# Optimization experiments

Measured on AMD Instinct MI355X. Metric: run time of the kernel, lower is better.

## Reference

```python
import jax, jax.numpy as jnp
import numpy as np

# SparseSphereConv (graph_level=6 -> V=40962, kernel_size=9, stride=1, select_index=None)
# Pipeline: neighbor gather -> data-dependent nonzero row selection ->
# per-vertex KxK interpolation matmul -> 1xK conv (linear over C_in,K) -> scatter back.
# With stride=1 / select_index=None the static selection is the identity, so the
# dynamic nonzero selection is equivalent to computing all rows and zeroing the
# rows whose gathered features are entirely zero (selected rows are scattered back,
# unselected rows stay 0 in sparse_reset's zero-initialized output).

BS, C_IN, C_OUT, V, K = 4, 32, 32, 40962, 9

def setup_inputs() -> dict:
    key = jax.random.key(0)
    k1, k2, k3, k4, k5 = jax.random.split(key, 5)
    x = jax.random.normal(k1, (BS, C_IN, V), dtype=jnp.float32)
    index = jax.random.randint(k2, (V, K), 0, V, dtype=jnp.int32)          # neighbor ids per vertex
    itp_mat = jax.random.uniform(k3, (V, K, K), dtype=jnp.float32)         # per-vertex interpolation
    conv_w = jax.random.normal(k4, (C_OUT, C_IN, K), dtype=jnp.float32) * 0.05  # Conv2d(C_in,C_out,(1,K)) weight
    conv_b = jax.random.normal(k5, (C_OUT,), dtype=jnp.float32) * 0.05
    return {"x": x, "index": index, "itp_mat": itp_mat, "conv_w": conv_w, "conv_b": conv_b}

def reference(x, index, itp_mat, conv_w, conv_b):
    # x: [bs, C, V] -> permute(2,0,1) -> gather neighbors -> [V, K, bs, C]
    g = jnp.transpose(x, (2, 0, 1))[index]
    g = jnp.transpose(g, (3, 2, 0, 1))                      # [C, bs, V, K]  (== reshape of [C, bs*V, K])
    # sparse_prepare: keep rows whose min or max over (C, K) is nonzero (detached in torch)
    gd = jax.lax.stop_gradient(g)
    rmin = gd.min(axis=(0, 3))                              # [bs, V]
    rmax = gd.max(axis=(0, 3))                              # [bs, V]
    mask = (rmin != 0) | (rmax != 0)                        # [bs, V]
    # Interploate: [C, S, 1, K] @ [S, K, K] per row -> batched small matmul
    interp = jnp.einsum('cbvk,vkj->cbvj', g, itp_mat)       # [C, bs, V, K]
    # Conv2d with kernel (1, K): contraction over (C_in, K) + bias
    out = jnp.einsum('cbvk,ock->bov', interp, conv_w) + conv_b[None, :, None]  # [bs, C_out, V]
    # sparse_reset: rows not selected stay zero
    return out * mask[:, None, :].astype(out.dtype)
```

## Files before the change

kernel.cpp:

```cpp
#include <hip/hip_runtime.h>
#include <hip/hip_bf16.h>

#define NV 40962
#define NK 9
#define CIN 32
#define COUT 32
#define NT 2561
#define NV81 (NV * 81)
#define NV9  (NV * 9)

typedef __attribute__((ext_vector_type(8))) short bf16x8;
typedef __attribute__((ext_vector_type(4))) float f32x4;
typedef __attribute__((ext_vector_type(2))) float f32x2;

#define PKFMA_L(A, G, R) asm("v_pk_fma_f32 %0, %1, %2, %0 op_sel:[0,0,0] op_sel_hi:[0,1,1]" : "+v"(A) : "v"(G), "v"(R))
#define PKFMA_H(A, G, R) asm("v_pk_fma_f32 %0, %1, %2, %0 op_sel:[1,0,0] op_sel_hi:[1,1,1]" : "+v"(A) : "v"(G), "v"(R))
#define PKMUL_L(A, G, R) asm("v_pk_mul_f32 %0, %1, %2 op_sel:[0,0] op_sel_hi:[0,1]" : "=v"(A) : "v"(G), "v"(R))
#define PKMUL_H(A, G, R) asm("v_pk_mul_f32 %0, %1, %2 op_sel:[1,0] op_sel_hi:[1,1]" : "=v"(A) : "v"(G), "v"(R))

#define ACC(cc, j) ((j) == 8 ? acc8[cc] : (((j) & 1) ? acc2[cc][(j) >> 1].y \
                                                     : acc2[cc][(j) >> 1].x))

__device__ __forceinline__ unsigned pkbf(float a, float b) {
    union { __hip_bfloat162 h2; unsigned u; } cv;
    cv.h2 = __float22bfloat162_rn(make_float2(a, b));
    return cv.u;
}

__global__ void __launch_bounds__(256) transpose_x_bf16(
    const float* __restrict__ x, unsigned* __restrict__ xtw,
    const float* __restrict__ w, unsigned short* __restrict__ wbf)
{
    __shared__ unsigned U[64 * 65];
    const int t = threadIdx.x;

    const int ci = blockIdx.x * 256 + t;
    if (ci < COUT * CIN * NK) {
        const int o = ci / 288;
        const int r = ci - o * 288;
        const int c = r / 9;
        const int j = r - c * 9;
        unsigned u = __float_as_uint(w[ci]);
        wbf[o * 288 + j * 32 + c] =
            (unsigned short)((u + 0x7FFFu + ((u >> 16) & 1u)) >> 16);
    }

    const int v0  = blockIdx.x * 64;
    const int l16 = t & 15;
    const int p   = t >> 4;

    #pragma unroll
    for (int i = 0; i < 4; ++i) {
        const int q    = p * 4 + i;
        const int r0   = 2 * q;
        const int bb   = r0 >> 5;
        const int c0   = r0 & 31;
        const int dwb  = (c0 >> 3) * 16 + bb * 4 + ((c0 & 7) >> 1);
        const float* rowA = x + (size_t)r0 * NV + v0;
        const float* rowB = rowA + NV;
        #pragma unroll
        for (int hv = 0; hv < 2; ++hv) {
            const int v = l16 * 2 + hv * 32;
            float2 a = make_float2(0.f, 0.f), c2 = make_float2(0.f, 0.f);
            if (v0 + v < NV) {
                a  = *(const float2*)(rowA + v);
                c2 = *(const float2*)(rowB + v);
            }
            U[(v    ) * 65 + dwb] = pkbf(a.x, c2.x);
            U[(v + 1) * 65 + dwb] = pkbf(a.y, c2.y);
        }
    }
    __syncthreads();

    const int v  = t >> 2;
    const int qo = t & 3;
    if (v0 + v < NV) {
        #pragma unroll
        for (int j = 0; j < 4; ++j) {
            const int n = j * 4 + qo;
            uint4 d;
            d.x = U[v * 65 + n * 4 + 0];
            d.y = U[v * 65 + n * 4 + 1];
            d.z = U[v * 65 + n * 4 + 2];
            d.w = U[v * 65 + n * 4 + 3];
            *(uint4*)&xtw[(size_t)(v0 + v) * 64 + n * 4] = d;
        }
    }
}

__global__ void __launch_bounds__(256, 2) sparse_conv_mfma(
    const unsigned short* __restrict__ xt, const int* __restrict__ index,
    const float* __restrict__ itp, const unsigned short* __restrict__ wbf,
    const float* __restrict__ bias, float* __restrict__ out)
{
    __shared__ float itp_s[4][4][108];

    const int t    = threadIdx.x;
    const int w    = t >> 6;
    const int lane = t & 63;
    const int arow = lane & 15;
    const int coct = lane >> 4;
    const int b    = (lane >> 2) & 3;
    const int vv   = lane & 3;
    const int tile = blockIdx.x;

    int ia = tile * 144 + w * 36 + (lane < 36 ? lane : 35);
    ia = ia < NV9 ? ia : NV9 - 1;
    const int myidx = index[ia];

    float iv[6];
    const size_t ibase = (size_t)(tile * 16 + w * 4) * 81;
    #pragma unroll
    for (int i = 0; i < 6; ++i) {
        const int o = i * 64 + lane;
        iv[i] = (o < 324 && ibase + o < (size_t)NV81) ? itp[ibase + o] : 0.0f;
    }

    const unsigned short* wb0 = wbf + arow * 288 + coct * 8;
    uint4 wa0[NK], wa1[NK];
    #pragma unroll
    for (int ks = 0; ks < NK; ++ks) {
        wa0[ks] = *(const uint4*)(wb0 + ks * 32);
        wa1[ks] = *(const uint4*)(wb0 + 16 * 288 + ks * 32);
    }

    float bs0[4], bs1[4];
    #pragma unroll
    for (int r = 0; r < 4; ++r) {
        bs0[r] = bias[coct * 4 + r];
        bs1[r] = bias[coct * 4 + 16 + r];
    }

    int nbr[NK];
    #pragma unroll
    for (int n = 0; n < NK; ++n) nbr[n] = __shfl(myidx, vv * 9 + n);
    const unsigned short* gbase = xt + coct * 32 + b * 8;
    uint4 g[NK];
    #pragma unroll
    for (int n = 0; n < NK; ++n)
        g[n] = *(const uint4*)(gbase + (size_t)nbr[n] * 128);

    #pragma unroll
    for (int i = 0; i < 6; ++i) {
        const int o = i * 64 + lane;
        if (o < 324) {
            const int vloc = o / 81;
            const int r2   = o - vloc * 81;
            const int kk   = r2 / 9;
            const int jj   = r2 - kk * 9;
            itp_s[w][vloc][kk * 12 + jj] = iv[i];
        }
    }
    __builtin_amdgcn_wave_barrier();

    unsigned frag[9][4];
    unsigned nzbits = 0;
    #pragma unroll
    for (int n = 0; n < NK; ++n)
        nzbits |= (g[n].x | g[n].y | g[n].z | g[n].w);
    nzbits &= 0x7FFF7FFFu;

    const float* ib = &itp_s[w][vv][0];
    #pragma unroll
    for (int h = 0; h < 2; ++h) {
        f32x2 acc2[4][4];
        float acc8[4];
        #pragma unroll
        for (int n = 0; n < NK; ++n) {
            const uint2 gk = h ? make_uint2(g[n].z, g[n].w)
                               : make_uint2(g[n].x, g[n].y);
            f32x2 gp01, gp23;
            gp01.x = __uint_as_float(gk.x << 16);
            gp01.y = __uint_as_float(gk.x & 0xFFFF0000u);
            gp23.x = __uint_as_float(gk.y << 16);
            gp23.y = __uint_as_float(gk.y & 0xFFFF0000u);
            const float* ir = ib + n * 12;
            const f32x4 ra = *(const f32x4*)ir;
            const f32x4 rb = *(const f32x4*)(ir + 4);
            const float r8 = ir[8];
            f32x2 rp[4];
            rp[0] = __builtin_shufflevector(ra, ra, 0, 1);
            rp[1] = __builtin_shufflevector(ra, ra, 2, 3);
            rp[2] = __builtin_shufflevector(rb, rb, 0, 1);
            rp[3] = __builtin_shufflevector(rb, rb, 2, 3);
            if (n == 0) {
                #pragma unroll
                for (int jp = 0; jp < 4; ++jp) {
                    PKMUL_L(acc2[0][jp], gp01, rp[jp]);
                    PKMUL_H(acc2[1][jp], gp01, rp[jp]);
                    PKMUL_L(acc2[2][jp], gp23, rp[jp]);
                    PKMUL_H(acc2[3][jp], gp23, rp[jp]);
                }
                acc8[0] = gp01.x * r8; acc8[1] = gp01.y * r8;
                acc8[2] = gp23.x * r8; acc8[3] = gp23.y * r8;
            } else {
                #pragma unroll
                for (int jp = 0; jp < 4; ++jp) {
                    PKFMA_L(acc2[0][jp], gp01, rp[jp]);
                    PKFMA_H(acc2[1][jp], gp01, rp[jp]);
                    PKFMA_L(acc2[2][jp], gp23, rp[jp]);
                    PKFMA_H(acc2[3][jp], gp23, rp[jp]);
                }
                acc8[0] += gp01.x * r8; acc8[1] += gp01.y * r8;
                acc8[2] += gp23.x * r8; acc8[3] += gp23.y * r8;
            }
        }
        #pragma unroll
        for (int ks = 0; ks < 9; ++ks) {
            frag[ks][2 * h]     = pkbf(ACC(0, ks), ACC(1, ks));
            frag[ks][2 * h + 1] = pkbf(ACC(2, ks), ACC(3, ks));
        }
    }

    unsigned nzw = nzbits;
    nzw |= __shfl_xor(nzw, 16);
    nzw |= __shfl_xor(nzw, 32);

    f32x4 c0 = {0.f, 0.f, 0.f, 0.f};
    f32x4 c1 = {0.f, 0.f, 0.f, 0.f};
    #pragma unroll
    for (int ks = 0; ks < 9; ++ks) {
        union { uint4 u; bf16x8 v; } bfr, au0, au1;
        bfr.u.x = frag[ks][0]; bfr.u.y = frag[ks][1];
        bfr.u.z = frag[ks][2]; bfr.u.w = frag[ks][3];
        au0.u = wa0[ks];
        au1.u = wa1[ks];
        c0 = __builtin_amdgcn_mfma_f32_16x16x32_bf16(au0.v, bfr.v, c0, 0, 0, 0);
        c1 = __builtin_amdgcn_mfma_f32_16x16x32_bf16(au1.v, bfr.v, c1, 0, 0, 0);
    }

    const int vglob = tile * 16 + w * 4 + vv;
    if (vglob < NV) {
        const float m = nzw ? 1.0f : 0.0f;
        float* ob = out + (size_t)b * (COUT * NV) + vglob;
        #pragma unroll
        for (int r = 0; r < 4; ++r) {
            ob[(size_t)(coct * 4 + r) * NV]      = (c0[r] + bs0[r]) * m;
            ob[(size_t)(coct * 4 + 16 + r) * NV] = (c1[r] + bs1[r]) * m;
        }
    }
}

extern "C" void kernel_launch(void* const* d_in, const int* in_sizes, int n_in,
                              void* d_out, int out_size, void* d_ws, size_t ws_size,
                              hipStream_t stream)
{
    const float* x     = (const float*)d_in[0];
    const int*   index = (const int*)  d_in[1];
    const float* itp   = (const float*)d_in[2];
    const float* w     = (const float*)d_in[3];
    const float* bias  = (const float*)d_in[4];
    float*       out   = (float*)d_out;

    unsigned short* xt  = (unsigned short*)d_ws;
    unsigned short* wbf = (unsigned short*)((char*)d_ws + (size_t)NV * 256);

    const int vchunks = (NV + 63) / 64;
    hipLaunchKernelGGL(transpose_x_bf16, dim3(vchunks), dim3(256), 0,
                       stream, x, (unsigned*)xt, w, wbf);
    hipLaunchKernelGGL(sparse_conv_mfma, dim3(NT), dim3(256), 0,
                       stream, xt, index, itp, wbf, bias, out);
}
```

Measured before the change: 124.2 us.

## Process two vertex tiles per block and prefetch second tile's gathers during first compute

Each block now handles two consecutive 16-vertex tiles, halving the grid. It loads index and interpolation data for both tiles up front, then issues the neighbor gathers for the second tile while the first tile's MFMA and stores run. The weight and bias register loads are amortized over two tiles. In exchange, register and LDS pressure rise under launch bounds of 2, and the halved grid gives fewer blocks to hide latency with.

```diff
diff --git a/kernel.cpp b/kernel.cpp
--- a/kernel.cpp
+++ b/kernel.cpp
@@ -6,6 +6,7 @@
 #define CIN 32
 #define COUT 32
 #define NT 2561
+#define NB2 1281
 #define NV81 (NV * 81)
 #define NV9  (NV * 9)
 
@@ -93,7 +94,7 @@
     const float* __restrict__ itp, const unsigned short* __restrict__ wbf,
     const float* __restrict__ bias, float* __restrict__ out)
 {
-    __shared__ float itp_s[4][4][108];
+    __shared__ float itp_s[4][2][4 * 108];
 
     const int t    = threadIdx.x;
     const int w    = t >> 6;
@@ -102,18 +103,31 @@
     const int coct = lane >> 4;
     const int b    = (lane >> 2) & 3;
     const int vv   = lane & 3;
-    const int tile = blockIdx.x;
-
-    int ia = tile * 144 + w * 36 + (lane < 36 ? lane : 35);
-    ia = ia < NV9 ? ia : NV9 - 1;
-    const int myidx = index[ia];
-
-    float iv[6];
-    const size_t ibase = (size_t)(tile * 16 + w * 4) * 81;
-    #pragma unroll
-    for (int i = 0; i < 6; ++i) {
-        const int o = i * 64 + lane;
-        iv[i] = (o < 324 && ibase + o < (size_t)NV81) ? itp[ibase + o] : 0.0f;
+    const int t0   = blockIdx.x * 2;
+    const int t1   = t0 + 1;
+    const bool vB  = (t1 < NT);
+
+    const int lidx = (lane < 36) ? lane : 35;
+
+    int iaA = t0 * 144 + w * 36 + lidx;
+    iaA = iaA < NV9 ? iaA : NV9 - 1;
+    const int myidxA = index[iaA];
+    int iaB = (vB ? t1 : t0) * 144 + w * 36 + lidx;
+    iaB = iaB < NV9 ? iaB : NV9 - 1;
+    const int myidxB = index[iaB];
+
+    float ivA[6], ivB[6];
+    {
+        const size_t baseA = (size_t)(t0 * 16 + w * 4) * 81;
+        const size_t baseB = (size_t)((vB ? t1 : t0) * 16 + w * 4) * 81;
+        #pragma unroll
+        for (int i = 0; i < 6; ++i) {
+            const int o = i * 64 + lane;
+            ivA[i] = (o < 324 && baseA + o < (size_t)NV81) ? itp[baseA + o]
+                                                           : 0.0f;
+            ivB[i] = (o < 324 && baseB + o < (size_t)NV81) ? itp[baseB + o]
+                                                           : 0.0f;
+        }
     }
 
     const unsigned short* wb0 = wbf + arow * 288 + coct * 8;
@@ -131,10 +145,10 @@
         bs1[r] = bias[coct * 4 + 16 + r];
     }
 
+    const unsigned short* gbase = xt + coct * 32 + b * 8;
     int nbr[NK];
     #pragma unroll
-    for (int n = 0; n < NK; ++n) nbr[n] = __shfl(myidx, vv * 9 + n);
-    const unsigned short* gbase = xt + coct * 32 + b * 8;
+    for (int n = 0; n < NK; ++n) nbr[n] = __shfl(myidxA, vv * 9 + n);
     uint4 g[NK];
     #pragma unroll
     for (int n = 0; n < NK; ++n)
@@ -148,95 +162,111 @@
             const int r2   = o - vloc * 81;
             const int kk   = r2 / 9;
             const int jj   = r2 - kk * 9;
-            itp_s[w][vloc][kk * 12 + jj] = iv[i];
+            itp_s[w][0][vloc * 108 + kk * 12 + jj] = ivA[i];
+            itp_s[w][1][vloc * 108 + kk * 12 + jj] = ivB[i];
         }
     }
     __builtin_amdgcn_wave_barrier();
 
+    f32x4 c0, c1;
     unsigned frag[9][4];
-    unsigned nzbits = 0;
-    #pragma unroll
-    for (int n = 0; n < NK; ++n)
-        nzbits |= (g[n].x | g[n].y | g[n].z | g[n].w);
-    nzbits &= 0x7FFF7FFFu;
-
-    const float* ib = &itp_s[w][vv][0];
-    #pragma unroll
-    for (int h = 0; h < 2; ++h) {
-        f32x2 acc2[4][4];
-        float acc8[4];
-        #pragma unroll
-        for (int n = 0; n < NK; ++n) {
-            const uint2 gk = h ? make_uint2(g[n].z, g[n].w)
-                               : make_uint2(g[n].x, g[n].y);
-            f32x2 gp01, gp23;
-            gp01.x = __uint_as_float(gk.x << 16);
-            gp01.y = __uint_as_float(gk.x & 0xFFFF0000u);
-            gp23.x = __uint_as_float(gk.y << 16);
-            gp23.y = __uint_as_float(gk.y & 0xFFFF0000u);
-            const float* ir = ib + n * 12;
-            const f32x4 ra = *(const f32x4*)ir;
-            const f32x4 rb = *(const f32x4*)(ir + 4);
-            const float r8 = ir[8];
-            f32x2 rp[4];
-            rp[0] = __builtin_shufflevector(ra, ra, 0, 1);
-            rp[1] = __builtin_shufflevector(ra, ra, 2, 3);
-            rp[2] = __builtin_shufflevector(rb, rb, 0, 1);
-            rp[3] = __builtin_shufflevector(rb, rb, 2, 3);
-            if (n == 0) {
-                #pragma unroll
-                for (int jp = 0; jp < 4; ++jp) {
-                    PKMUL_L(acc2[0][jp], gp01, rp[jp]);
-                    PKMUL_H(acc2[1][jp], gp01, rp[jp]);
-                    PKMUL_L(acc2[2][jp], gp23, rp[jp]);
-                    PKMUL_H(acc2[3][jp], gp23, rp[jp]);
+
+    #pragma unroll
+    for (int tt = 0; tt < 2; ++tt) {
+        if (tt == 1 && !vB) break;
+
+        unsigned nzbits = 0;
+        #pragma unroll
+        for (int n = 0; n < NK; ++n)
+            nzbits |= (g[n].x | g[n].y | g[n].z | g[n].w);
+        nzbits &= 0x7FFF7FFFu;
+
+        const float* ib = &itp_s[w][tt][vv * 108];
+        #pragma unroll
+        for (int h = 0; h < 2; ++h) {
+            f32x2 acc2[4][4];
+            float acc8[4];
+            #pragma unroll
+            for (int n = 0; n < NK; ++n) {
+                const uint2 gk = h ? make_uint2(g[n].z, g[n].w)
+                                   : make_uint2(g[n].x, g[n].y);
+                f32x2 gp01, gp23;
+                gp01.x = __uint_as_float(gk.x << 16);
+                gp01.y = __uint_as_float(gk.x & 0xFFFF0000u);
+                gp23.x = __uint_as_float(gk.y << 16);
+                gp23.y = __uint_as_float(gk.y & 0xFFFF0000u);
+                const float* ir = ib + n * 12;
+                const f32x4 ra = *(const f32x4*)ir;
+                const f32x4 rb = *(const f32x4*)(ir + 4);
+                const float r8 = ir[8];
+                f32x2 rp[4];
+                rp[0] = __builtin_shufflevector(ra, ra, 0, 1);
+                rp[1] = __builtin_shufflevector(ra, ra, 2, 3);
+                rp[2] = __builtin_shufflevector(rb, rb, 0, 1);
+                rp[3] = __builtin_shufflevector(rb, rb, 2, 3);
+                if (n == 0) {
+                    #pragma unroll
+                    for (int jp = 0; jp < 4; ++jp) {
+                        PKMUL_L(acc2[0][jp], gp01, rp[jp]);
+                        PKMUL_H(acc2[1][jp], gp01, rp[jp]);
+                        PKMUL_L(acc2[2][jp], gp23, rp[jp]);
+                        PKMUL_H(acc2[3][jp], gp23, rp[jp]);
+                    }
+                    acc8[0] = gp01.x * r8; acc8[1] = gp01.y * r8;
+                    acc8[2] = gp23.x * r8; acc8[3] = gp23.y * r8;
+                } else {
+                    #pragma unroll
+                    for (int jp = 0; jp < 4; ++jp) {
+                        PKFMA_L(acc2[0][jp], gp01, rp[jp]);
+                        PKFMA_H(acc2[1][jp], gp01, rp[jp]);
+                        PKFMA_L(acc2[2][jp], gp23, rp[jp]);
+                        PKFMA_H(acc2[3][jp], gp23, rp[jp]);
+                    }
+                    acc8[0] += gp01.x * r8; acc8[1] += gp01.y * r8;
+                    acc8[2] += gp23.x * r8; acc8[3] += gp23.y * r8;
                 }
-                acc8[0] = gp01.x * r8; acc8[1] = gp01.y * r8;
-                acc8[2] = gp23.x * r8; acc8[3] = gp23.y * r8;
-            } else {
-                #pragma unroll
-                for (int jp = 0; jp < 4; ++jp) {
-                    PKFMA_L(acc2[0][jp], gp01, rp[jp]);
-                    PKFMA_H(acc2[1][jp], gp01, rp[jp]);
-                    PKFMA_L(acc2[2][jp], gp23, rp[jp]);
-                    PKFMA_H(acc2[3][jp], gp23, rp[jp]);
-                }
-                acc8[0] += gp01.x * r8; acc8[1] += gp01.y * r8;
-                acc8[2] += gp23.x * r8; acc8[3] += gp23.y * r8;
-            }
-        }
+            }
+            #pragma unroll
+            for (int ks = 0; ks < 9; ++ks) {
+                frag[ks][2 * h]     = pkbf(ACC(0, ks), ACC(1, ks));
+                frag[ks][2 * h + 1] = pkbf(ACC(2, ks), ACC(3, ks));
+            }
+        }
+
+        if (tt == 0 && vB) {
+            #pragma unroll
+            for (int n = 0; n < NK; ++n) nbr[n] = __shfl(myidxB, vv * 9 + n);
+            #pragma unroll
+            for (int n = 0; n < NK; ++n)
+                g[n] = *(const uint4*)(gbase + (size_t)nbr[n] * 128);
+        }
+
+        unsigned nzw = nzbits;
+        nzw |= __shfl_xor(nzw, 16);
+        nzw |= __shfl_xor(nzw, 32);
+
+        c0 = (f32x4){0.f, 0.f, 0.f, 0.f};
+        c1 = (f32x4){0.f, 0.f, 0.f, 0.f};
         #pragma unroll
         for (int ks = 0; ks < 9; ++ks) {
-            frag[ks][2 * h]     = pkbf(ACC(0, ks), ACC(1, ks));
-            frag[ks][2 * h + 1] = pkbf(ACC(2, ks), ACC(3, ks));
-        }
-    }
-
-    unsigned nzw = nzbits;
-    nzw |= __shfl_xor(nzw, 16);
-    nzw |= __shfl_xor(nzw, 32);
-
-    f32x4 c0 = {0.f, 0.f, 0.f, 0.f};
-    f32x4 c1 = {0.f, 0.f, 0.f, 0.f};
-    #pragma unroll
-    for (int ks = 0; ks < 9; ++ks) {
-        union { uint4 u; bf16x8 v; } bfr, au0, au1;
-        bfr.u.x = frag[ks][0]; bfr.u.y = frag[ks][1];
-        bfr.u.z = frag[ks][2]; bfr.u.w = frag[ks][3];
-        au0.u = wa0[ks];
-        au1.u = wa1[ks];
-        c0 = __builtin_amdgcn_mfma_f32_16x16x32_bf16(au0.v, bfr.v, c0, 0, 0, 0);
-        c1 = __builtin_amdgcn_mfma_f32_16x16x32_bf16(au1.v, bfr.v, c1, 0, 0, 0);
-    }
-
-    const int vglob = tile * 16 + w * 4 + vv;
-    if (vglob < NV) {
-        const float m = nzw ? 1.0f : 0.0f;
-        float* ob = out + (size_t)b * (COUT * NV) + vglob;
-        #pragma unroll
-        for (int r = 0; r < 4; ++r) {
-            ob[(size_t)(coct * 4 + r) * NV]      = (c0[r] + bs0[r]) * m;
-            ob[(size_t)(coct * 4 + 16 + r) * NV] = (c1[r] + bs1[r]) * m;
+            union { uint4 u; bf16x8 v; } bfr, au0, au1;
+            bfr.u.x = frag[ks][0]; bfr.u.y = frag[ks][1];
+            bfr.u.z = frag[ks][2]; bfr.u.w = frag[ks][3];
+            au0.u = wa0[ks];
+            au1.u = wa1[ks];
+            c0 = __builtin_amdgcn_mfma_f32_16x16x32_bf16(au0.v, bfr.v, c0, 0, 0, 0);
+            c1 = __builtin_amdgcn_mfma_f32_16x16x32_bf16(au1.v, bfr.v, c1, 0, 0, 0);
+        }
+
+        const int vglob = (t0 + tt) * 16 + w * 4 + vv;
+        if (vglob < NV) {
+            const float m = nzw ? 1.0f : 0.0f;
+            float* ob = out + (size_t)b * (COUT * NV) + vglob;
+            #pragma unroll
+            for (int r = 0; r < 4; ++r) {
+                ob[(size_t)(coct * 4 + r) * NV]      = (c0[r] + bs0[r]) * m;
+                ob[(size_t)(coct * 4 + 16 + r) * NV] = (c1[r] + bs1[r]) * m;
+            }
         }
     }
 }
@@ -258,6 +288,6 @@
     const int vchunks = (NV + 63) / 64;
     hipLaunchKernelGGL(transpose_x_bf16, dim3(vchunks), dim3(256), 0,
                        stream, x, (unsigned*)xt, w, wbf);
-    hipLaunchKernelGGL(sparse_conv_mfma, dim3(NT), dim3(256), 0,
+    hipLaunchKernelGGL(sparse_conv_mfma, dim3(NB2), dim3(256), 0,
                        stream, xt, index, itp, wbf, bias, out);
 }
```

Result: slower. 165.3 us (+33.1%).
